# Performance work log

Hardware: AMD Instinct MI355X
Metric: run time of the kernel (lower is better)

Reference implementation:

```python
import jax, jax.numpy as jnp
import numpy as np
from jax import lax

D_MODEL = 384
D_INNER = 768   # expand * d_model
D_STATE = 16
DT_RANK = 24
K_CONV = 4
B_SZ = 2
L_SEQ = 2048


def setup_inputs() -> dict:
    key = jax.random.key(0)
    ks = jax.random.split(key, 11)
    inp = {}
    inp["x"] = jax.random.normal(ks[0], (B_SZ, L_SEQ, D_MODEL), dtype=jnp.float32)
    # learned parameters (Mamba block)
    inp["in_proj_w"] = jax.random.normal(ks[1], (D_MODEL, 2 * D_INNER), dtype=jnp.float32) * 0.02
    inp["conv_w"] = jax.random.normal(ks[2], (D_INNER, K_CONV), dtype=jnp.float32) * 0.1
    inp["conv_b"] = jnp.zeros((D_INNER,), dtype=jnp.float32)
    inp["x_proj_w"] = jax.random.normal(ks[3], (D_INNER, DT_RANK + 2 * D_STATE), dtype=jnp.float32) * 0.02
    inp["dt_proj_w"] = jax.random.normal(ks[4], (DT_RANK, D_INNER), dtype=jnp.float32) * 0.1
    inp["dt_proj_b"] = jnp.full((D_INNER,), -2.0, dtype=jnp.float32)  # softplus(-2) ~ small init dt
    # A_log initialized so A = -exp(A_log) = -[1..d_state]
    inp["A_log"] = jnp.log(jnp.broadcast_to(jnp.arange(1, D_STATE + 1, dtype=jnp.float32), (D_INNER, D_STATE)))
    inp["D"] = jnp.ones((D_INNER,), dtype=jnp.float32)
    inp["out_proj_w"] = jax.random.normal(ks[5], (D_INNER, D_MODEL), dtype=jnp.float32) * 0.02
    return inp


def _silu(x):
    return x * jax.nn.sigmoid(x)


def reference(x, in_proj_w, conv_w, conv_b, x_proj_w, dt_proj_w, dt_proj_b, A_log, D, out_proj_w):
    B, L, _ = x.shape
    d_inner, n = A_log.shape
    k = conv_w.shape[-1]

    # input projection and gate split
    xz = jnp.einsum("bld,de->ble", x, in_proj_w)          # [B, L, 2*d_inner]
    xp, z = jnp.split(xz, 2, axis=-1)                       # each [B, L, d_inner]

    # causal depthwise 1D conv along sequence
    xp_t = xp.transpose(0, 2, 1)                            # [B, d_inner, L]
    conv_out = lax.conv_general_dilated(
        xp_t, conv_w[:, None, :],                           # kernel [O=d_inner, I/g=1, K]
        window_strides=(1,), padding=[(k - 1, 0)],
        dimension_numbers=("NCH", "OIH", "NCH"),
        feature_group_count=d_inner,
    ) + conv_b[None, :, None]
    xp = _silu(conv_out.transpose(0, 2, 1))                 # [B, L, d_inner]

    # data-dependent SSM parameters
    x_dbl = jnp.einsum("bld,de->ble", xp, x_proj_w)         # [B, L, dt_rank + 2n]
    dt_r = x_dbl[..., :DT_RANK]
    Bm = x_dbl[..., DT_RANK:DT_RANK + n]                    # [B, L, n]
    Cm = x_dbl[..., DT_RANK + n:]                           # [B, L, n]
    dt = jax.nn.softplus(jnp.einsum("blr,rd->bld", dt_r, dt_proj_w) + dt_proj_b)  # [B, L, d_inner]

    A = -jnp.exp(A_log)                                     # [d_inner, n]
    dA = jnp.exp(jnp.einsum("bld,dn->bldn", dt, A))         # discretized state transition
    dBx = jnp.einsum("bln,bld->bldn", Bm, dt * xp)          # input contribution

    # sequential selective scan over L
    def step(h, inputs):
        dA_t, dBx_t, C_t = inputs                           # [B,d,n],[B,d,n],[B,n]
        h = dA_t * h + dBx_t
        y = jnp.einsum("bdn,bn->bd", h, C_t)
        return h, y

    h0 = jnp.zeros((B, d_inner, n), dtype=x.dtype)
    _, ys = lax.scan(step, h0, (dA.transpose(1, 0, 2, 3), dBx.transpose(1, 0, 2, 3), Cm.transpose(1, 0, 2)))
    y = ys.transpose(1, 0, 2)                               # [B, L, d_inner]

    y = y + xp * D                                          # skip term
    y = y * _silu(z)                                        # gating
    return jnp.einsum("bld,de->ble", y, out_proj_w)         # [B, L, d_model]
```

## Files before the change

### kernel.cpp

```cpp
#include <hip/hip_runtime.h>
#include <hip/hip_bf16.h>

#define B_SZ    2
#define L_SEQ   2048
#define D_MODEL 384
#define D_INNER 768
#define D_STATE 16
#define DT_RANK 24
#define ML      (B_SZ * L_SEQ)
#define NCHUNK  64
#define CHLEN   (L_SEQ / NCHUNK)

typedef __hip_bfloat16 bf16;
typedef __attribute__((ext_vector_type(8))) short bf16x8;
typedef __attribute__((ext_vector_type(4))) float f32x4;
typedef __attribute__((ext_vector_type(8))) float f32x8;

__global__ __launch_bounds__(256)
void gemm_inproj(const float* __restrict__ Af, const float* __restrict__ W,
                 const float* __restrict__ xpw, const float* __restrict__ opw,
                 bf16* __restrict__ outb0, bf16* __restrict__ outb1,
                 float* __restrict__ xdbl_zero, float* __restrict__ dout_zero,
                 bf16* __restrict__ Wtx, bf16* __restrict__ Wto)
{
    __shared__ __attribute__((aligned(16))) short As[64][72];
    __shared__ __attribute__((aligned(16))) short Bs[64][72];
    const int tid  = threadIdx.x;

    {
        int gidx = (blockIdx.y * gridDim.x + blockIdx.x) * 256 + tid;
        f32x4 z;
        z[0] = 0.f; z[1] = 0.f; z[2] = 0.f; z[3] = 0.f;
        *(f32x4*)&dout_zero[(size_t)gidx * 4] = z;
        if (gidx < ML * 56) xdbl_zero[gidx] = 0.f;
        if (gidx < D_MODEL * D_INNER) {
            int n = gidx / D_INNER, k = gidx - n * D_INNER;
            Wto[gidx] = __float2bfloat16(opw[(size_t)k * D_MODEL + n]);
        } else if (gidx < D_MODEL * D_INNER + 56 * D_INNER) {
            int g2 = gidx - D_MODEL * D_INNER;
            int n = g2 / D_INNER, k = g2 - n * D_INNER;
            Wtx[g2] = __float2bfloat16(xpw[(size_t)k * 56 + n]);
        }
    }

    const int lane = tid & 63;
    const int wave = tid >> 6;
    const int wm   = (wave & 1) * 32;
    const int wn   = (wave >> 1) * 32;
    const int m0   = blockIdx.y * 64;
    const int n0   = blockIdx.x * 64;
    const int N    = 2 * D_INNER;
    const int K    = D_MODEL;

    f32x4 acc[2][2];
#pragma unroll
    for (int i = 0; i < 2; i++)
#pragma unroll
        for (int j = 0; j < 2; j++)
#pragma unroll
            for (int r = 0; r < 4; r++) acc[i][j][r] = 0.f;

    for (int kt = 0; kt < K; kt += 64) {
        __syncthreads();
#pragma unroll
        for (int i = 0; i < 2; i++) {
            int c = tid + 256 * i;
            int m = c >> 3, k8 = (c & 7) * 8;
            f32x8 a = *(const f32x8*)&Af[(size_t)(m0 + m) * K + kt + k8];
            bf16x8 h;
#pragma unroll
            for (int j = 0; j < 8; j++)
                h[j] = (short)__bfloat16_as_ushort(__float2bfloat16(a[j]));
            *(bf16x8*)&As[m][k8] = h;
        }
#pragma unroll
        for (int i = 0; i < 2; i++) {
            int c = tid + 256 * i;
            int n8 = (c & 7) * 8, k = c >> 3;
            f32x8 w = *(const f32x8*)&W[(size_t)(kt + k) * N + n0 + n8];
#pragma unroll
            for (int j = 0; j < 8; j++)
                Bs[n8 + j][k] = (short)__bfloat16_as_ushort(__float2bfloat16(w[j]));
        }
        __syncthreads();
#pragma unroll
        for (int ks = 0; ks < 2; ks++) {
            int kb = ks * 32 + (lane >> 4) * 8;
            bf16x8 a0 = *(const bf16x8*)&As[wm + (lane & 15)][kb];
            bf16x8 a1 = *(const bf16x8*)&As[wm + 16 + (lane & 15)][kb];
            bf16x8 b0 = *(const bf16x8*)&Bs[wn + (lane & 15)][kb];
            bf16x8 b1 = *(const bf16x8*)&Bs[wn + 16 + (lane & 15)][kb];
            acc[0][0] = __builtin_amdgcn_mfma_f32_16x16x32_bf16(a0, b0, acc[0][0], 0, 0, 0);
            acc[0][1] = __builtin_amdgcn_mfma_f32_16x16x32_bf16(a0, b1, acc[0][1], 0, 0, 0);
            acc[1][0] = __builtin_amdgcn_mfma_f32_16x16x32_bf16(a1, b0, acc[1][0], 0, 0, 0);
            acc[1][1] = __builtin_amdgcn_mfma_f32_16x16x32_bf16(a1, b1, acc[1][1], 0, 0, 0);
        }
    }

    const bool zside = (n0 >= D_INNER);
    __syncthreads();
#pragma unroll
    for (int am = 0; am < 2; am++)
#pragma unroll
        for (int bn = 0; bn < 2; bn++)
#pragma unroll
            for (int r = 0; r < 4; r++) {
                int ml = wm + am * 16 + (lane >> 4) * 4 + r;
                int nl = wn + bn * 16 + (lane & 15);
                float v = acc[am][bn][r];
                if (zside) v = v / (1.f + __expf(-v));
                As[nl][ml] = (short)__bfloat16_as_ushort(__float2bfloat16(v));
            }
    __syncthreads();
    {
        bf16* outp = zside ? (outb1 + (size_t)(n0 - D_INNER) * ML)
                           : (outb0 + (size_t)n0 * ML);
#pragma unroll
        for (int i = 0; i < 2; i++) {
            int idx = tid + 256 * i;
            int nl = idx >> 3, m8 = (idx & 7) * 8;
            bf16x8 vrow = *(const bf16x8*)&As[nl][m8];
            *(bf16x8*)&outp[(size_t)nl * ML + m0 + m8] = vrow;
        }
    }
}

__global__ __launch_bounds__(256)
void gemm_xproj_conv(const bf16* __restrict__ Xraw, const bf16* __restrict__ Wtx,
                     const float* __restrict__ cw, const float* __restrict__ cb,
                     bf16* __restrict__ xp_t, float* __restrict__ outf)
{
    __shared__ __attribute__((aligned(16))) short As[64][72];
    __shared__ __attribute__((aligned(16))) short Bs[64][72];
    const int tid  = threadIdx.x;
    const int lane = tid & 63;
    const int wave = tid >> 6;
    const int wm   = (wave & 1) * 32;
    const int wn   = (wave >> 1) * 32;
    const int m0   = blockIdx.y * 64;
    const int k0   = blockIdx.x * (768 / 4);
    const int N    = 56;

    f32x4 acc[2][2];
#pragma unroll
    for (int i = 0; i < 2; i++)
#pragma unroll
        for (int j = 0; j < 2; j++)
#pragma unroll
            for (int r = 0; r < 4; r++) acc[i][j][r] = 0.f;

    for (int kt = k0; kt < k0 + 192; kt += 64) {
        __syncthreads();
#pragma unroll
        for (int i = 0; i < 2; i++) {
            int c = tid + 256 * i;
            int m8 = (c & 7) * 8, k = c >> 3;
            const int d  = kt + k;
            const size_t row = (size_t)d * ML;
            const int mg = m0 + m8;
            const int l0 = mg & (L_SEQ - 1);

            bf16x8 cur = *(const bf16x8*)&Xraw[row + mg];
            bf16x8 prev;
            if (mg != 0) prev = *(const bf16x8*)&Xraw[row + mg - 8];
            else {
#pragma unroll
                for (int j = 0; j < 8; j++) prev[j] = 0;
            }
            const float w0 = cw[d * 4 + 0], w1 = cw[d * 4 + 1],
                        w2 = cw[d * 4 + 2], w3 = cw[d * 4 + 3], bias = cb[d];
            float wv[16];
#pragma unroll
            for (int j = 0; j < 8; j++) {
                wv[j]     = __uint_as_float(((unsigned)(unsigned short)prev[j]) << 16);
                wv[j + 8] = __uint_as_float(((unsigned)(unsigned short)cur[j]) << 16);
            }
            bf16x8 out;
#pragma unroll
            for (int o = 0; o < 8; o++) {
                int l = l0 + o;
                float s = bias;
                if (l >= 3) {
                    s += w0 * wv[5 + o] + w1 * wv[6 + o] + w2 * wv[7 + o] + w3 * wv[8 + o];
                } else {
                    if (l - 3 >= 0) s += w0 * wv[5 + o];
                    if (l - 2 >= 0) s += w1 * wv[6 + o];
                    if (l - 1 >= 0) s += w2 * wv[7 + o];
                    s += w3 * wv[8 + o];
                }
                float act = s / (1.f + __expf(-s));
                out[o] = (short)__bfloat16_as_ushort(__float2bfloat16(act));
                As[m8 + o][k] = out[o];
            }
            *(bf16x8*)&xp_t[row + mg] = out;
        }
#pragma unroll
        for (int i = 0; i < 2; i++) {
            int c = tid + 256 * i;
            int n = c >> 3, k8 = (c & 7) * 8;
            if (n < N) {
                *(bf16x8*)&Bs[n][k8] =
                    *(const bf16x8*)&Wtx[(size_t)n * D_INNER + kt + k8];
            } else {
                bf16x8 zz;
#pragma unroll
                for (int j = 0; j < 8; j++) zz[j] = 0;
                *(bf16x8*)&Bs[n][k8] = zz;
            }
        }
        __syncthreads();
#pragma unroll
        for (int ks = 0; ks < 2; ks++) {
            int kb = ks * 32 + (lane >> 4) * 8;
            bf16x8 a0 = *(const bf16x8*)&As[wm + (lane & 15)][kb];
            bf16x8 a1 = *(const bf16x8*)&As[wm + 16 + (lane & 15)][kb];
            bf16x8 b0 = *(const bf16x8*)&Bs[wn + (lane & 15)][kb];
            bf16x8 b1 = *(const bf16x8*)&Bs[wn + 16 + (lane & 15)][kb];
            acc[0][0] = __builtin_amdgcn_mfma_f32_16x16x32_bf16(a0, b0, acc[0][0], 0, 0, 0);
            acc[0][1] = __builtin_amdgcn_mfma_f32_16x16x32_bf16(a0, b1, acc[0][1], 0, 0, 0);
            acc[1][0] = __builtin_amdgcn_mfma_f32_16x16x32_bf16(a1, b0, acc[1][0], 0, 0, 0);
            acc[1][1] = __builtin_amdgcn_mfma_f32_16x16x32_bf16(a1, b1, acc[1][1], 0, 0, 0);
        }
    }

#pragma unroll
    for (int am = 0; am < 2; am++)
#pragma unroll
        for (int bn = 0; bn < 2; bn++)
#pragma unroll
            for (int r = 0; r < 4; r++) {
                int m = m0 + wm + am * 16 + (lane >> 4) * 4 + r;
                int n = wn + bn * 16 + (lane & 15);
                if (n < N)
                    atomicAdd(&outf[(size_t)m * N + n], acc[am][bn][r]);
            }
}

__global__ __launch_bounds__(256)
void gemm_outproj_split(const bf16* __restrict__ At, const bf16* __restrict__ Wto,
                        float* __restrict__ outf)
{
    __shared__ __attribute__((aligned(16))) short As[64][72];
    __shared__ __attribute__((aligned(16))) short Bs[64][72];
    const int tid  = threadIdx.x;
    const int lane = tid & 63;
    const int wave = tid >> 6;
    const int wm   = (wave & 1) * 32;
    const int wn   = (wave >> 1) * 32;
    const int n0   = blockIdx.x * 64;
    const int m0   = blockIdx.y * 64;
    const int k0   = blockIdx.z * (768 / 4);

    f32x4 acc[2][2];
#pragma unroll
    for (int i = 0; i < 2; i++)
#pragma unroll
        for (int j = 0; j < 2; j++)
#pragma unroll
            for (int r = 0; r < 4; r++) acc[i][j][r] = 0.f;

    for (int kt = k0; kt < k0 + 192; kt += 64) {
        __syncthreads();
#pragma unroll
        for (int i = 0; i < 2; i++) {
            int c = tid + 256 * i;
            int m8 = (c & 7) * 8, k = c >> 3;
            bf16x8 a = *(const bf16x8*)&At[(size_t)(kt + k) * ML + m0 + m8];
#pragma unroll
            for (int j = 0; j < 8; j++) As[m8 + j][k] = a[j];
        }
#pragma unroll
        for (int i = 0; i < 2; i++) {
            int c = tid + 256 * i;
            int n = c >> 3, k8 = (c & 7) * 8;
            *(bf16x8*)&Bs[n][k8] =
                *(const bf16x8*)&Wto[(size_t)(n0 + n) * D_INNER + kt + k8];
        }
        __syncthreads();
#pragma unroll
        for (int ks = 0; ks < 2; ks++) {
            int kb = ks * 32 + (lane >> 4) * 8;
            bf16x8 a0 = *(const bf16x8*)&As[wm + (lane & 15)][kb];
            bf16x8 a1 = *(const bf16x8*)&As[wm + 16 + (lane & 15)][kb];
            bf16x8 b0 = *(const bf16x8*)&Bs[wn + (lane & 15)][kb];
            bf16x8 b1 = *(const bf16x8*)&Bs[wn + 16 + (lane & 15)][kb];
            acc[0][0] = __builtin_amdgcn_mfma_f32_16x16x32_bf16(a0, b0, acc[0][0], 0, 0, 0);
            acc[0][1] = __builtin_amdgcn_mfma_f32_16x16x32_bf16(a0, b1, acc[0][1], 0, 0, 0);
            acc[1][0] = __builtin_amdgcn_mfma_f32_16x16x32_bf16(a1, b0, acc[1][0], 0, 0, 0);
            acc[1][1] = __builtin_amdgcn_mfma_f32_16x16x32_bf16(a1, b1, acc[1][1], 0, 0, 0);
        }
    }

#pragma unroll
    for (int am = 0; am < 2; am++)
#pragma unroll
        for (int bn = 0; bn < 2; bn++)
#pragma unroll
            for (int r = 0; r < 4; r++) {
                int m = m0 + wm + am * 16 + (lane >> 4) * 4 + r;
                int n = n0 + wn + bn * 16 + (lane & 15);
                atomicAdd(&outf[(size_t)m * D_MODEL + n], acc[am][bn][r]);
            }
}

__global__ __launch_bounds__(256)
void dt_kernel(const float* __restrict__ x_dbl, const float* __restrict__ dtw,
               const float* __restrict__ dtb, bf16* __restrict__ dt_t)
{
    const int tid  = threadIdx.x;
    const int lane = tid & 63;
    const int wv   = __builtin_amdgcn_readfirstlane(tid >> 6);
    const int m    = blockIdx.x * 64 + lane;
    const int d0   = blockIdx.y * 48 + wv * 12;

    float xs[24];
    {
        const float* rowp = &x_dbl[(size_t)m * 56];
        f32x8 v0 = *(const f32x8*)&rowp[0];
        f32x8 v1 = *(const f32x8*)&rowp[8];
        f32x8 v2 = *(const f32x8*)&rowp[16];
#pragma unroll
        for (int j = 0; j < 8; j++) {
            xs[j] = v0[j]; xs[8 + j] = v1[j]; xs[16 + j] = v2[j];
        }
    }

#pragma unroll
    for (int i = 0; i < 12; i++) {
        const int dd = d0 + i;
        float acc = dtb[dd];
#pragma unroll
        for (int r = 0; r < 24; r++)
            acc += xs[r] * dtw[r * D_INNER + dd];
        float sp = fmaxf(acc, 0.f) + log1pf(__expf(-fabsf(acc)));
        dt_t[(size_t)dd * ML + m] = __float2bfloat16(sp);
    }
}

__global__ __launch_bounds__(1024)
void scan_kernel(const bf16* __restrict__ dt_t, const bf16* __restrict__ xp_t,
                 const float* __restrict__ x_dbl, const bf16* __restrict__ zs_t,
                 const float* __restrict__ A_log, const float* __restrict__ Dp,
                 bf16* __restrict__ y_t)
{
    __shared__ float sP[NCHUNK][D_STATE + 1];
    __shared__ float sH[NCHUNK][D_STATE + 1];
    const int tid = threadIdx.x;
    const int c = tid >> 4;
    const int n = tid & 15;
    const int g = blockIdx.x;
    const int b = g / D_INNER;
    const int d = g % D_INNER;
    const float A = -__expf(A_log[d * D_STATE + n]);
    const size_t base_t = (size_t)d * ML + (size_t)b * L_SEQ + (size_t)c * CHLEN;
    const size_t base_m = (size_t)b * L_SEQ + (size_t)c * CHLEN;

    float h = 0.f, P = 1.f;
#pragma unroll
    for (int g2 = 0; g2 < 2; g2++) {
        bf16x8 vdt0 = *(const bf16x8*)&dt_t[base_t + g2 * 16];
        bf16x8 vdt1 = *(const bf16x8*)&dt_t[base_t + g2 * 16 + 8];
        bf16x8 vxp0 = *(const bf16x8*)&xp_t[base_t + g2 * 16];
        bf16x8 vxp1 = *(const bf16x8*)&xp_t[base_t + g2 * 16 + 8];
#pragma unroll
        for (int k = 0; k < 16; k++) {
            const int j = g2 * 16 + k;
            short sdt = (k < 8) ? vdt0[k & 7] : vdt1[k & 7];
            short sxp = (k < 8) ? vxp0[k & 7] : vxp1[k & 7];
            float dtv = __uint_as_float(((unsigned)(unsigned short)sdt) << 16);
            float xpv = __uint_as_float(((unsigned)(unsigned short)sxp) << 16);
            float Bn  = x_dbl[(base_m + j) * 56 + DT_RANK + n];
            float aj = __expf(dtv * A);
            h = aj * h + Bn * (dtv * xpv);
            P *= aj;
        }
    }
    sP[c][n] = P;
    sH[c][n] = h;
    __syncthreads();

    {
        const int wv = tid >> 6;
        const int ln = tid & 63;
        float p = sP[ln][wv];
        float hh = sH[ln][wv];
#pragma unroll
        for (int s = 1; s < NCHUNK; s <<= 1) {
            float p2 = __shfl_up(p, s);
            float h2 = __shfl_up(hh, s);
            if (ln >= s) { hh = p * h2 + hh; p = p * p2; }
        }
        sP[ln][wv] = p;
        sH[ln][wv] = hh;
    }
    __syncthreads();
    const float hinit = (c == 0) ? 0.f : sH[c - 1][n];

    const float Dd = Dp[d];
    h = hinit;
#pragma unroll
    for (int g2 = 0; g2 < 2; g2++) {
        bf16x8 vdt0 = *(const bf16x8*)&dt_t[base_t + g2 * 16];
        bf16x8 vdt1 = *(const bf16x8*)&dt_t[base_t + g2 * 16 + 8];
        bf16x8 vxp0 = *(const bf16x8*)&xp_t[base_t + g2 * 16];
        bf16x8 vxp1 = *(const bf16x8*)&xp_t[base_t + g2 * 16 + 8];
        float ymine = 0.f, xmine = 0.f;
#pragma unroll
        for (int k = 0; k < 16; k++) {
            const int j = g2 * 16 + k;
            short sdt = (k < 8) ? vdt0[k & 7] : vdt1[k & 7];
            short sxp = (k < 8) ? vxp0[k & 7] : vxp1[k & 7];
            float dtv = __uint_as_float(((unsigned)(unsigned short)sdt) << 16);
            float xpv = __uint_as_float(((unsigned)(unsigned short)sxp) << 16);
            float Bn  = x_dbl[(base_m + j) * 56 + DT_RANK + n];
            float aj = __expf(dtv * A);
            h = aj * h + Bn * (dtv * xpv);
            float Cn = x_dbl[(base_m + j) * 56 + DT_RANK + D_STATE + n];
            float yv = h * Cn;
            yv += __shfl_xor(yv, 1);
            yv += __shfl_xor(yv, 2);
            yv += __shfl_xor(yv, 4);
            yv += __shfl_xor(yv, 8);
            ymine = (k == n) ? yv : ymine;
            xmine = (k == n) ? xpv : xmine;
        }
        const int j = g2 * 16 + n;
        float zsv = __bfloat162float(zs_t[base_t + j]);
        y_t[base_t + j] = __float2bfloat16((ymine + xmine * Dd) * zsv);
    }
}

extern "C" void kernel_launch(void* const* d_in, const int* in_sizes, int n_in,
                              void* d_out, int out_size, void* d_ws, size_t ws_size,
                              hipStream_t stream)
{
    const float* x         = (const float*)d_in[0];
    const float* in_proj_w = (const float*)d_in[1];
    const float* conv_w    = (const float*)d_in[2];
    const float* conv_b    = (const float*)d_in[3];
    const float* x_proj_w  = (const float*)d_in[4];
    const float* dt_proj_w = (const float*)d_in[5];
    const float* dt_proj_b = (const float*)d_in[6];
    const float* A_log     = (const float*)d_in[7];
    const float* Dvec      = (const float*)d_in[8];
    const float* out_proj_w= (const float*)d_in[9];

    bf16* xp_raw_t = (bf16*)d_ws;
    bf16* zs_t     = xp_raw_t + (size_t)ML * D_INNER;
    bf16* xp_t     = zs_t     + (size_t)ML * D_INNER;
    bf16* dt_t     = xp_t     + (size_t)ML * D_INNER;
    float* x_dbl   = (float*)(dt_t + (size_t)ML * D_INNER);
    bf16* Wto      = (bf16*)(x_dbl + (size_t)ML * 56);
    bf16* Wtx      = Wto + (size_t)D_MODEL * D_INNER;
    bf16* y_t      = xp_raw_t;

    dim3 blk(256);

    gemm_inproj<<<dim3(2 * D_INNER / 64, ML / 64), blk, 0, stream>>>(
        x, in_proj_w, x_proj_w, out_proj_w, xp_raw_t, zs_t, x_dbl, (float*)d_out,
        Wtx, Wto);

    gemm_xproj_conv<<<dim3(4, ML / 64), blk, 0, stream>>>(
        xp_raw_t, Wtx, conv_w, conv_b, xp_t, x_dbl);

    dt_kernel<<<dim3(ML / 64, D_INNER / 48), blk, 0, stream>>>(
        x_dbl, dt_proj_w, dt_proj_b, dt_t);

    scan_kernel<<<B_SZ * D_INNER, 1024, 0, stream>>>(
        dt_t, xp_t, x_dbl, zs_t, A_log, Dvec, y_t);

    gemm_outproj_split<<<dim3(D_MODEL / 64, ML / 64, 4), blk, 0, stream>>>(
        y_t, Wto, (float*)d_out);
}
```

Baseline: 221.1 us.

## Fuse dt projection into x_proj GEMM via last-block-done counter

Removes the separate dt_kernel launch by having the last of the four split-K blocks for each 64-row tile compute the dt projection and softplus. A per-row-tile atomic counter, zeroed in the in_proj kernel, identifies that last block, and it reads x_dbl with acquire loads. This saves a launch and a round of x_dbl reads, but the dt work now runs on only 64 blocks, each looping over 192 output channels per wave, so there is much less parallelism than the old dt_kernel grid had. The dt_t stores are also less coalesced.

```diff
diff --git a/kernel.cpp b/kernel.cpp
--- a/kernel.cpp
+++ b/kernel.cpp
@@ -21,7 +21,8 @@
                  const float* __restrict__ xpw, const float* __restrict__ opw,
                  bf16* __restrict__ outb0, bf16* __restrict__ outb1,
                  float* __restrict__ xdbl_zero, float* __restrict__ dout_zero,
-                 bf16* __restrict__ Wtx, bf16* __restrict__ Wto)
+                 bf16* __restrict__ Wtx, bf16* __restrict__ Wto,
+                 unsigned int* __restrict__ dcnt)
 {
     __shared__ __attribute__((aligned(16))) short As[64][72];
     __shared__ __attribute__((aligned(16))) short Bs[64][72];
@@ -33,6 +34,7 @@
         z[0] = 0.f; z[1] = 0.f; z[2] = 0.f; z[3] = 0.f;
         *(f32x4*)&dout_zero[(size_t)gidx * 4] = z;
         if (gidx < ML * 56) xdbl_zero[gidx] = 0.f;
+        if (gidx < 64) dcnt[gidx] = 0u;
         if (gidx < D_MODEL * D_INNER) {
             int n = gidx / D_INNER, k = gidx - n * D_INNER;
             Wto[gidx] = __float2bfloat16(opw[(size_t)k * D_MODEL + n]);
@@ -128,10 +130,13 @@
 __global__ __launch_bounds__(256)
 void gemm_xproj_conv(const bf16* __restrict__ Xraw, const bf16* __restrict__ Wtx,
                      const float* __restrict__ cw, const float* __restrict__ cb,
-                     bf16* __restrict__ xp_t, float* __restrict__ outf)
+                     const float* __restrict__ dtw, const float* __restrict__ dtb,
+                     bf16* __restrict__ xp_t, float* __restrict__ x_dbl,
+                     bf16* __restrict__ dt_t, unsigned int* __restrict__ dcnt)
 {
     __shared__ __attribute__((aligned(16))) short As[64][72];
     __shared__ __attribute__((aligned(16))) short Bs[64][72];
+    __shared__ int sLast;
     const int tid  = threadIdx.x;
     const int lane = tid & 63;
     const int wave = tid >> 6;
@@ -232,8 +237,35 @@
                 int m = m0 + wm + am * 16 + (lane >> 4) * 4 + r;
                 int n = wn + bn * 16 + (lane & 15);
                 if (n < N)
-                    atomicAdd(&outf[(size_t)m * N + n], acc[am][bn][r]);
-            }
+                    atomicAdd(&x_dbl[(size_t)m * N + n], acc[am][bn][r]);
+            }
+
+    __threadfence();
+    __syncthreads();
+    if (tid == 0) {
+        unsigned prev = atomicAdd(&dcnt[blockIdx.y], 1u);
+        sLast = (prev == 3u);
+    }
+    __syncthreads();
+    if (sLast) {
+        __threadfence();
+        const int m = m0 + lane;
+        float xs[24];
+#pragma unroll
+        for (int r = 0; r < 24; r++)
+            xs[r] = __hip_atomic_load(&x_dbl[(size_t)m * 56 + r],
+                                      __ATOMIC_ACQUIRE, __HIP_MEMORY_SCOPE_AGENT);
+        const int wvq = __builtin_amdgcn_readfirstlane(wave);
+        for (int i = 0; i < 192; i++) {
+            const int dd = wvq * 192 + i;
+            float a2 = dtb[dd];
+#pragma unroll
+            for (int r = 0; r < 24; r++)
+                a2 += xs[r] * dtw[r * D_INNER + dd];
+            float sp = fmaxf(a2, 0.f) + log1pf(__expf(-fabsf(a2)));
+            dt_t[(size_t)dd * ML + m] = __float2bfloat16(sp);
+        }
+    }
 }
 
 __global__ __launch_bounds__(256)
@@ -301,40 +333,6 @@
                 int n = n0 + wn + bn * 16 + (lane & 15);
                 atomicAdd(&outf[(size_t)m * D_MODEL + n], acc[am][bn][r]);
             }
-}
-
-__global__ __launch_bounds__(256)
-void dt_kernel(const float* __restrict__ x_dbl, const float* __restrict__ dtw,
-               const float* __restrict__ dtb, bf16* __restrict__ dt_t)
-{
-    const int tid  = threadIdx.x;
-    const int lane = tid & 63;
-    const int wv   = __builtin_amdgcn_readfirstlane(tid >> 6);
-    const int m    = blockIdx.x * 64 + lane;
-    const int d0   = blockIdx.y * 48 + wv * 12;
-
-    float xs[24];
-    {
-        const float* rowp = &x_dbl[(size_t)m * 56];
-        f32x8 v0 = *(const f32x8*)&rowp[0];
-        f32x8 v1 = *(const f32x8*)&rowp[8];
-        f32x8 v2 = *(const f32x8*)&rowp[16];
-#pragma unroll
-        for (int j = 0; j < 8; j++) {
-            xs[j] = v0[j]; xs[8 + j] = v1[j]; xs[16 + j] = v2[j];
-        }
-    }
-
-#pragma unroll
-    for (int i = 0; i < 12; i++) {
-        const int dd = d0 + i;
-        float acc = dtb[dd];
-#pragma unroll
-        for (int r = 0; r < 24; r++)
-            acc += xs[r] * dtw[r * D_INNER + dd];
-        float sp = fmaxf(acc, 0.f) + log1pf(__expf(-fabsf(acc)));
-        dt_t[(size_t)dd * ML + m] = __float2bfloat16(sp);
-    }
 }
 
 __global__ __launch_bounds__(1024)
@@ -452,19 +450,18 @@
     float* x_dbl   = (float*)(dt_t + (size_t)ML * D_INNER);
     bf16* Wto      = (bf16*)(x_dbl + (size_t)ML * 56);
     bf16* Wtx      = Wto + (size_t)D_MODEL * D_INNER;
+    unsigned int* dcnt = (unsigned int*)(Wtx + (size_t)56 * D_INNER);
     bf16* y_t      = xp_raw_t;
 
     dim3 blk(256);
 
     gemm_inproj<<<dim3(2 * D_INNER / 64, ML / 64), blk, 0, stream>>>(
         x, in_proj_w, x_proj_w, out_proj_w, xp_raw_t, zs_t, x_dbl, (float*)d_out,
-        Wtx, Wto);
+        Wtx, Wto, dcnt);
 
     gemm_xproj_conv<<<dim3(4, ML / 64), blk, 0, stream>>>(
-        xp_raw_t, Wtx, conv_w, conv_b, xp_t, x_dbl);
-
-    dt_kernel<<<dim3(ML / 64, D_INNER / 48), blk, 0, stream>>>(
-        x_dbl, dt_proj_w, dt_proj_b, dt_t);
+        xp_raw_t, Wtx, conv_w, conv_b, dt_proj_w, dt_proj_b, xp_t, x_dbl,
+        dt_t, dcnt);
 
     scan_kernel<<<B_SZ * D_INNER, 1024, 0, stream>>>(
         dt_t, xp_t, x_dbl, zs_t, A_log, Dvec, y_t);
```

Result: slower. 381.3 us (+72.5%).
